# Kernel optimization log

Hardware: AMD Instinct MI355X
Metric: run time of the kernel (lower is better)

## Reference

```python
import jax, jax.numpy as jnp
import numpy as np

B, S, D = 2, 8192, 1024
H, DK, DV = 8, 64, 64
DH = 4096
SEG = 2048
NSEG = S // SEG
EPS = 1e-5


def setup_inputs() -> dict:
    key = jax.random.key(0)
    ks = jax.random.split(key, 9)
    g = lambda k, shp, sc: jax.random.normal(k, shp, jnp.float32) * sc
    return {
        "x": g(ks[0], (B, S, D), 1.0),
        "Wq": g(ks[1], (D, H * DK), 0.02),
        "Wk": g(ks[2], (D, H * DK), 0.02),
        "Wv": g(ks[3], (D, H * DV), 0.02),
        "Wo": g(ks[4], (H * DV, D), 0.02),
        "betas": g(ks[5], (1, H, 1, DV), 1.0),
        "W1": g(ks[6], (D, DH), 0.02),
        "b1": jnp.zeros((DH,), jnp.float32),
        "W2": g(ks[7], (DH, D), 0.02),
        "b2": jnp.zeros((D,), jnp.float32),
        "ln_g": jnp.ones((D,), jnp.float32),
        "ln_b": jnp.zeros((D,), jnp.float32),
    }


def _compressive_memory(x, Wq, Wk, Wv, Wo, betas):
    # project and split heads: (B, H, S, d)
    q = (x @ Wq).reshape(B, S, H, DK).transpose(0, 2, 1, 3)
    k = (x @ Wk).reshape(B, S, H, DK).transpose(0, 2, 1, 3)
    v = (x @ Wv).reshape(B, S, H, DV).transpose(0, 2, 1, 3)

    # chunk into segments: (NSEG, B, H, SEG, d)
    seg = lambda t, d: t.reshape(B, H, NSEG, SEG, d).transpose(2, 0, 1, 3, 4)
    qs, ks_, vs = seg(q, DK), seg(k, DK), seg(v, DV)

    mem0 = jnp.zeros((B, H, DK, DV), jnp.float32)
    z0 = jnp.ones((B, H, DK, 1), jnp.float32) / DK
    causal_mask = jnp.tril(jnp.ones((SEG, SEG), bool))
    scale = np.float32(1.0 / np.sqrt(DK))
    gate = jax.nn.sigmoid(betas)  # (1, H, 1, DV)

    def step(carry, inp):
        mem, z = carry
        qi, ki, vi = inp  # (B, H, SEG, d)
        sq = jax.nn.elu(qi) + 1.0
        sk = jax.nn.elu(ki) + 1.0
        # memory retrieval (uses state from previous segments)
        att_mem = (sq @ mem) / (sq @ z)  # (B, H, SEG, DV)
        # local causal SDP attention within the segment
        scores = jnp.einsum('bhqd,bhkd->bhqk', qi, ki) * scale
        scores = jnp.where(causal_mask, scores, -jnp.inf)
        att_dot = jax.nn.softmax(scores, axis=-1) @ vi
        # linear memory update
        mem = mem + jnp.einsum('bhsd,bhsv->bhdv', sk, vi)
        z = z + sk.sum(axis=-2, keepdims=True).transpose(0, 1, 3, 2)
        att = gate * att_mem + (1.0 - gate) * att_dot
        return (mem, z), att

    _, atts = jax.lax.scan(step, (mem0, z0), (qs, ks_, vs))
    # (NSEG, B, H, SEG, DV) -> (B, S, H*DV)
    att = atts.transpose(1, 0, 3, 2, 4).reshape(B, S, H * DV)
    return att @ Wo


def reference(x, Wq, Wk, Wv, Wo, betas, W1, b1, W2, b2, ln_g, ln_b):
    a = _compressive_memory(x, Wq, Wk, Wv, Wo, betas)
    h = jax.nn.gelu(a @ W1 + b1, approximate=False) @ W2 + b2
    y = h + x
    mu = y.mean(axis=-1, keepdims=True)
    var = ((y - mu) ** 2).mean(axis=-1, keepdims=True)
    return (y - mu) / jnp.sqrt(var + EPS) * ln_g + ln_b
```

## Files before the change

### kernel.cpp

```cpp
#include <hip/hip_runtime.h>
#include <hip/hip_bf16.h>
#include <math.h>

#define B_    2
#define S_    8192
#define D_    1024
#define H_N   8
#define DK_   64
#define DV_   64
#define DH_   4096
#define SEG_  2048
#define NSEG_ 4
#define EPS_  1e-5f
#define LDQKV 1536

typedef __hip_bfloat16 bf16;
typedef unsigned int u32;
typedef __attribute__((ext_vector_type(8))) short bf16x8;
typedef __attribute__((ext_vector_type(4))) float f32x4;

union bvec { bf16x8 v; bf16 e[8]; };

template <typename T> __device__ inline T from_f(float v);
template <> __device__ inline float from_f<float>(float v) { return v; }
template <> __device__ inline bf16  from_f<bf16>(float v)  { return __float2bfloat16(v); }

__device__ __forceinline__ void gld_lds16(const bf16* g, bf16* l) {
    __builtin_amdgcn_global_load_lds(
        (const __attribute__((address_space(1))) u32*)g,
        (__attribute__((address_space(3))) u32*)l, 16, 0, 0);
}

__device__ inline float elu1(float x) { return x > 0.f ? x + 1.f : __expf(x); }

template <int EPI, typename CT>
__global__ __launch_bounds__(512, 2) void gemm256(
    const bf16* __restrict__ A, const bf16* __restrict__ BT, CT* __restrict__ C,
    const float* __restrict__ bias, const float* __restrict__ resid,
    int M, int N, int K)
{
    __shared__ bf16 L[4][16384];
    const int t    = threadIdx.x;
    const int lane = t & 63;
    const int w    = t >> 6;
    const int la   = lane & 15;
    const int g    = lane >> 4;

    const int nx  = gridDim.x;
    const int nwg = nx * gridDim.y;
    const int lin = blockIdx.y * nx + blockIdx.x;
    const int swz = (lin & 7) * (nwg >> 3) + (lin >> 3);
    const int by  = swz / nx, bx = swz - by * nx;

    const int m0 = by * 256, n0 = bx * 256;
    const int wm = w >> 2, wn = w & 3;

    f32x4 acc[8][4];
    #pragma unroll
    for (int m = 0; m < 8; m++)
        #pragma unroll
        for (int n = 0; n < 4; n++) {
            f32x4 z4 = {0.f, 0.f, 0.f, 0.f};
            acc[m][n] = z4;
        }

    const bf16* Aw = A  + (size_t)(m0 + w * 32) * K;
    const bf16* Bw = BT + (size_t)(n0 + w * 32) * K;
    const int rl = lane >> 2;
    const int co = (((lane & 3) ^ ((lane >> 3) & 3))) * 8;

    const int nt = K >> 5;

    auto stage = [&](int kt) {
        const int buf = kt & 3;
        const int k0 = kt << 5;
        #pragma unroll
        for (int i = 0; i < 2; i++) {
            gld_lds16(Aw + (size_t)(i * 16 + rl) * K + k0 + co,
                      &L[buf][(w * 32 + i * 16) * 32]);
            gld_lds16(Bw + (size_t)(i * 16 + rl) * K + k0 + co,
                      &L[buf][8192 + (w * 32 + i * 16) * 32]);
        }
    };

    stage(0);
    stage(1);
    asm volatile("s_waitcnt vmcnt(4)" ::: "memory");
    __builtin_amdgcn_s_barrier();

    for (int kt = 0; kt < nt; kt++) {
        const int buf = kt & 3;
        if (kt + 2 < nt) stage(kt + 2);

        const bf16* Ab_ = &L[buf][0];
        const bf16* Bb_ = &L[buf][8192];
        const int rsw = (la >> 1) & 3;
        bf16x8 af[8], bg[4];
        #pragma unroll
        for (int m = 0; m < 8; m++) {
            int row = wm * 128 + m * 16 + la;
            af[m] = *(const bf16x8*)&Ab_[row * 32 + 8 * (g ^ rsw)];
        }
        #pragma unroll
        for (int n = 0; n < 4; n++) {
            int row = wn * 64 + n * 16 + la;
            bg[n] = *(const bf16x8*)&Bb_[row * 32 + 8 * (g ^ rsw)];
        }

        __builtin_amdgcn_s_setprio(1);
        #pragma unroll
        for (int m = 0; m < 8; m++)
            #pragma unroll
            for (int n = 0; n < 4; n++)
                acc[m][n] = __builtin_amdgcn_mfma_f32_16x16x32_bf16(
                    af[m], bg[n], acc[m][n], 0, 0, 0);
        __builtin_amdgcn_s_setprio(0);

        if (kt + 1 < nt) {
            if (kt + 2 < nt) asm volatile("s_waitcnt vmcnt(4)" ::: "memory");
            else             asm volatile("s_waitcnt vmcnt(0)" ::: "memory");
            __builtin_amdgcn_sched_barrier(0);
            __builtin_amdgcn_s_barrier();
        }
    }

    const int row0 = m0 + wm * 128 + g * 4;
    const int col0 = n0 + wn * 64 + la;
    #pragma unroll
    for (int n = 0; n < 4; n++) {
        const int col = col0 + n * 16;
        const float bj = (EPI >= 2) ? bias[col] : 0.f;
        #pragma unroll
        for (int m = 0; m < 8; m++) {
            #pragma unroll
            for (int r = 0; r < 4; r++) {
                const int row = row0 + m * 16 + r;
                float v = acc[m][n][r];
                if (EPI >= 2) v += bj;
                if (EPI == 2) v = 0.5f * v * (1.0f + erff(v * 0.70710678118654752f));
                if (EPI == 3) v += resid[(size_t)row * N + col];
                C[(size_t)row * N + col] = from_f<CT>(v);
            }
        }
    }
}

__global__ __launch_bounds__(256) void castx_k(const float* __restrict__ X,
                                               bf16* __restrict__ Y)
{
    size_t i = ((size_t)blockIdx.x * 256 + threadIdx.x) * 4;
    float4 v = *(const float4*)(X + i);
    union { bf16 b[4]; unsigned long long u; } o;
    o.b[0] = __float2bfloat16(v.x);
    o.b[1] = __float2bfloat16(v.y);
    o.b[2] = __float2bfloat16(v.z);
    o.b[3] = __float2bfloat16(v.w);
    *(unsigned long long*)(Y + i) = o.u;
}

__global__ __launch_bounds__(256) void transcast_k(const float* __restrict__ W,
                                                   bf16* __restrict__ WT, int K, int N)
{
    __shared__ float tile[32][33];
    const int n0 = blockIdx.x * 32, k0 = blockIdx.y * 32;
    const int tx = threadIdx.x & 31, ty = threadIdx.x >> 5;
    #pragma unroll
    for (int i = 0; i < 32; i += 8)
        tile[ty + i][tx] = W[(size_t)(k0 + ty + i) * N + n0 + tx];
    __syncthreads();
    #pragma unroll
    for (int i = 0; i < 32; i += 8)
        WT[(size_t)(n0 + ty + i) * K + k0 + tx] = __float2bfloat16(tile[tx][ty + i]);
}

__global__ __launch_bounds__(256) void vtrans_k(const bf16* __restrict__ V,
                                                bf16* __restrict__ Vt)
{
    __shared__ bf16 t_[64 * 64];
    const int t = threadIdx.x;
    const int sblk = blockIdx.x & 127;
    const int b = blockIdx.x >> 7;
    const int h = blockIdx.y;
    const bf16* src = V + ((size_t)b * S_ + sblk * 64) * LDQKV + h * 64;
    #pragma unroll
    for (int k = 0; k < 2; k++) {
        int e = t + k * 256;
        int r = e >> 3, c8 = (e & 7) * 8;
        *(bf16x8*)&t_[r * 64 + c8] = *(const bf16x8*)&src[(size_t)r * LDQKV + c8];
    }
    __syncthreads();
    const int dv = t & 63, s0 = (t >> 6) * 16;
    bf16* dst = Vt + ((size_t)(b * 8 + h) * 64 + dv) * (size_t)S_ + sblk * 64 + s0;
    bvec o0, o1;
    #pragma unroll
    for (int i = 0; i < 8; i++) {
        o0.e[i] = t_[(s0 + i) * 64 + dv];
        o1.e[i] = t_[(s0 + 8 + i) * 64 + dv];
    }
    *(bf16x8*)dst = o0.v;
    *(bf16x8*)(dst + 8) = o1.v;
}

__global__ __launch_bounds__(256) void memseg_k(
    const bf16* __restrict__ Kg, const bf16* __restrict__ Vg,
    float* __restrict__ MP, float* __restrict__ ZP)
{
    __shared__ float Ks[64][65];
    __shared__ float Vs[64][65];
    const int t = threadIdx.x, tx = t & 15, ty = t >> 4;
    const int sb = blockIdx.x;
    const int seg = sb >> 4, bh = sb & 15;
    const int b = bh >> 3, h = bh & 7;
    const int chunk = blockIdx.y;
    const size_t base = ((size_t)b * S_ + (size_t)seg * SEG_ + (size_t)chunk * 512) * LDQKV + h * 64;

    float acc[4][4] = {};
    float zacc[4]   = {};
    for (int st = 0; st < 8; st++) {
        #pragma unroll
        for (int kk = 0; kk < 2; kk++) {
            int e = t + kk * 256;
            int r = e >> 3, c8 = (e & 7) * 8;
            size_t go = base + ((size_t)st * 64 + r) * LDQKV + c8;
            bvec kv_, vv_;
            kv_.v = *(const bf16x8*)&Kg[go];
            vv_.v = *(const bf16x8*)&Vg[go];
            #pragma unroll
            for (int i = 0; i < 8; i++) {
                Ks[r][c8 + i] = elu1(__bfloat162float(kv_.e[i]));
                Vs[r][c8 + i] = __bfloat162float(vv_.e[i]);
            }
        }
        __syncthreads();
        for (int s = 0; s < 64; s++) {
            float a4[4], v4[4];
            #pragma unroll
            for (int i = 0; i < 4; i++) a4[i] = Ks[s][ty * 4 + i];
            #pragma unroll
            for (int j = 0; j < 4; j++) v4[j] = Vs[s][tx * 4 + j];
            #pragma unroll
            for (int i = 0; i < 4; i++)
                #pragma unroll
                for (int j = 0; j < 4; j++)
                    acc[i][j] += a4[i] * v4[j];
        }
        #pragma unroll
        for (int ii = 0; ii < 4; ii++) {
            int s = tx + ii * 16;
            #pragma unroll
            for (int i = 0; i < 4; i++) zacc[i] += Ks[s][ty * 4 + i];
        }
        __syncthreads();
    }
    const int slot = (seg * 4 + chunk) * 16 + bh;
    #pragma unroll
    for (int i = 0; i < 4; i++)
        #pragma unroll
        for (int j = 0; j < 4; j++)
            MP[(size_t)slot * 4096 + (ty * 4 + i) * 64 + tx * 4 + j] = acc[i][j];
    #pragma unroll
    for (int i = 0; i < 4; i++) {
        float zz = zacc[i];
        #pragma unroll
        for (int mk = 1; mk < 16; mk <<= 1) zz += __shfl_xor(zz, mk);
        if (tx == 0) ZP[slot * 64 + ty * 4 + i] = zz;
    }
}

__global__ __launch_bounds__(256) void prefix_k(
    const float* __restrict__ MP, const float* __restrict__ ZP,
    bf16* __restrict__ MST, float* __restrict__ ZS)
{
    const int bh = blockIdx.x, t = threadIdx.x;
    for (int e = t; e < 4096; e += 256) {
        int dk = e >> 6, dv = e & 63;
        float s = 0.f;
        #pragma unroll
        for (int slot = 0; slot < 16; slot++) {
            if ((slot & 3) == 0)
                MST[(size_t)((slot >> 2) * 16 + bh) * 4096 + dv * 64 + dk] = __float2bfloat16(s);
            s += MP[(size_t)(slot * 16 + bh) * 4096 + e];
        }
    }
    if (t < 64) {
        float s = 1.0f / DK_;
        #pragma unroll
        for (int slot = 0; slot < 16; slot++) {
            if ((slot & 3) == 0) ZS[((slot >> 2) * 16 + bh) * 64 + t] = s;
            s += ZP[(slot * 16 + bh) * 64 + t];
        }
    }
}

template <int NG>
__device__ __forceinline__ void stageT(const bf16* gsrc, size_t stride, bf16* lds,
                                       int wave, int lane)
{
    #pragma unroll
    for (int ii = 0; ii < NG; ii++) {
        int i = wave * NG + ii;
        gld_lds16(gsrc + (size_t)(8 * i + (lane >> 3)) * stride
                        + (size_t)(((lane & 7) ^ (lane >> 3)) * 8),
                  lds + i * 512);
    }
}

__device__ __forceinline__ bf16x8 ldsw128(const bf16* base, int row, int colE)
{
    int off = row * 128 + ((colE * 2) ^ ((row & 7) << 4));
    return *(const bf16x8*)((const char*)base + off);
}

__global__ __launch_bounds__(256) void attn_k(
    const bf16* __restrict__ Qg, const bf16* __restrict__ Kg, const bf16* __restrict__ Vt,
    const bf16* __restrict__ MsT, const float* __restrict__ ZS,
    const float* __restrict__ betas, bf16* __restrict__ att)
{
    __shared__ bf16 KT[2][4096];
    __shared__ bf16 VTs[2][4096];
    __shared__ bf16 QP[8192];
    __shared__ float Zsm[64];

    const int t    = threadIdx.x;
    const int lane = t & 63;
    const int w    = t >> 6;
    const int la   = lane & 15;
    const int g    = lane >> 4;
    const int qt   = (int)gridDim.x - 1 - (int)blockIdx.x;
    const int bh   = blockIdx.y;
    const int seg  = blockIdx.z;
    const int b    = bh >> 3, h = bh & 7;

    const size_t srow = (size_t)b * S_ + (size_t)seg * SEG_;
    const bf16* qp  = Qg + (srow + (size_t)qt * 128) * LDQKV + h * 64;
    const bf16* kp  = Kg + srow * LDQKV + h * 64;
    const bf16* vtp = Vt + (size_t)bh * 64 * (size_t)S_ + (size_t)seg * SEG_;

    stageT<4>(qp, LDQKV, QP, w, lane);
    stageT<2>(kp, LDQKV, KT[0], w, lane);
    stageT<2>(vtp, S_, VTs[0], w, lane);
    if (t < 64) Zsm[t] = ZS[(seg * 16 + bh) * 64 + t];
    __syncthreads();

    bf16x8 aq[2][2];
    #pragma unroll
    for (int st = 0; st < 2; st++)
        #pragma unroll
        for (int s = 0; s < 2; s++)
            aq[st][s] = ldsw128(QP, w * 32 + st * 16 + la, s * 32 + g * 8);

    float m_[2] = {-1e30f, -1e30f};
    float l_[2] = {0.f, 0.f};
    f32x4 Oa[2][4];
    #pragma unroll
    for (int st = 0; st < 2; st++)
        #pragma unroll
        for (int j = 0; j < 4; j++) { f32x4 z4 = {0.f,0.f,0.f,0.f}; Oa[st][j] = z4; }

    const int jtmax = 2 * qt + 1;
    int cur = 0;
    for (int jt = 0; jt <= jtmax; jt++, cur ^= 1) {
        if (jt < jtmax) {
            stageT<2>(kp + (size_t)(jt + 1) * 64 * LDQKV, LDQKV, KT[cur ^ 1], w, lane);
            stageT<2>(vtp + (size_t)(jt + 1) * 64, S_, VTs[cur ^ 1], w, lane);
        }

        bf16x8 kf[2][4];
        #pragma unroll
        for (int s = 0; s < 2; s++)
            #pragma unroll
            for (int j = 0; j < 4; j++)
                kf[s][j] = ldsw128(KT[cur], j * 16 + la, s * 32 + g * 8);

        const int jtkv = jt * 64;
        #pragma unroll
        for (int st = 0; st < 2; st++) {
            f32x4 sc[4];
            #pragma unroll
            for (int j = 0; j < 4; j++) { f32x4 z4 = {0.f,0.f,0.f,0.f}; sc[j] = z4; }
            #pragma unroll
            for (int j = 0; j < 4; j++) {
                sc[j] = __builtin_amdgcn_mfma_f32_16x16x32_bf16(kf[0][j], aq[st][0], sc[j], 0, 0, 0);
                sc[j] = __builtin_amdgcn_mfma_f32_16x16x32_bf16(kf[1][j], aq[st][1], sc[j], 0, 0, 0);
            }

            const int q_abs = qt * 128 + w * 32 + st * 16 + la;
            float sv[4][4];
            float mx = -1e30f;
            #pragma unroll
            for (int j = 0; j < 4; j++)
                #pragma unroll
                for (int r = 0; r < 4; r++) {
                    float v = sc[j][r] * 0.125f;
                    int kv = jtkv + j * 16 + g * 4 + r;
                    v = (kv <= q_abs) ? v : -1e30f;
                    sv[j][r] = v;
                    mx = fmaxf(mx, v);
                }
            mx = fmaxf(mx, __shfl_xor(mx, 16));
            mx = fmaxf(mx, __shfl_xor(mx, 32));
            float mnew = fmaxf(m_[st], mx);
            float corr = __expf(m_[st] - mnew);
            float rs = 0.f;
            #pragma unroll
            for (int j = 0; j < 4; j++)
                #pragma unroll
                for (int r = 0; r < 4; r++) {
                    float p = __expf(sv[j][r] - mnew);
                    sv[j][r] = p;
                    rs += p;
                }
            rs += __shfl_xor(rs, 16);
            rs += __shfl_xor(rs, 32);
            l_[st] = l_[st] * corr + rs;
            m_[st] = mnew;

            const int R = w * 32 + st * 16 + la;
            #pragma unroll
            for (int j = 0; j < 4; j++) {
                union { bf16 e[4]; uint2 u; } pk;
                #pragma unroll
                for (int r = 0; r < 4; r++) pk.e[r] = __float2bfloat16(sv[j][r]);
                int off = R * 128 + ((j * 32 + g * 8) ^ ((la & 7) << 4));
                *(uint2*)((char*)QP + off) = pk.u;
            }

            #pragma unroll
            for (int r = 0; r < 4; r++) {
                float corr_r = __shfl(corr, (lane & 48) | (g * 4 + r));
                #pragma unroll
                for (int j = 0; j < 4; j++) Oa[st][j][r] *= corr_r;
            }
        }

        asm volatile("s_waitcnt lgkmcnt(0)" ::: "memory");
        __builtin_amdgcn_sched_barrier(0);

        bf16x8 bv[2][4];
        #pragma unroll
        for (int s = 0; s < 2; s++)
            #pragma unroll
            for (int j = 0; j < 4; j++)
                bv[s][j] = ldsw128(VTs[cur], j * 16 + la, s * 32 + g * 8);
        #pragma unroll
        for (int st = 0; st < 2; st++) {
            bf16x8 ap0 = ldsw128(QP, w * 32 + st * 16 + la, g * 8);
            bf16x8 ap1 = ldsw128(QP, w * 32 + st * 16 + la, 32 + g * 8);
            #pragma unroll
            for (int j = 0; j < 4; j++) {
                Oa[st][j] = __builtin_amdgcn_mfma_f32_16x16x32_bf16(ap0, bv[0][j], Oa[st][j], 0, 0, 0);
                Oa[st][j] = __builtin_amdgcn_mfma_f32_16x16x32_bf16(ap1, bv[1][j], Oa[st][j], 0, 0, 0);
            }
        }
        __syncthreads();
    }

    stageT<2>(MsT + (size_t)(seg * 16 + bh) * 4096, 64, KT[0], w, lane);
    __syncthreads();

    bf16x8 sq[2][2];
    float den[2] = {0.f, 0.f};
    #pragma unroll
    for (int st = 0; st < 2; st++) {
        #pragma unroll
        for (int s = 0; s < 2; s++) {
            bvec in, outv;
            in.v = aq[st][s];
            #pragma unroll
            for (int e = 0; e < 8; e++) {
                float f = elu1(__bfloat162float(in.e[e]));
                outv.e[e] = __float2bfloat16(f);
                den[st] += f * Zsm[s * 32 + g * 8 + e];
            }
            sq[st][s] = outv.v;
        }
        den[st] += __shfl_xor(den[st], 16);
        den[st] += __shfl_xor(den[st], 32);
    }

    bf16x8 bm[2][4];
    #pragma unroll
    for (int s = 0; s < 2; s++)
        #pragma unroll
        for (int j = 0; j < 4; j++)
            bm[s][j] = ldsw128(KT[0], j * 16 + la, s * 32 + g * 8);

    float gate[4];
    #pragma unroll
    for (int j = 0; j < 4; j++)
        gate[j] = 1.f / (1.f + __expf(-betas[h * 64 + j * 16 + la]));

    #pragma unroll
    for (int st = 0; st < 2; st++) {
        f32x4 num[4];
        #pragma unroll
        for (int j = 0; j < 4; j++) { f32x4 z4 = {0.f,0.f,0.f,0.f}; num[j] = z4; }
        #pragma unroll
        for (int j = 0; j < 4; j++) {
            num[j] = __builtin_amdgcn_mfma_f32_16x16x32_bf16(sq[st][0], bm[0][j], num[j], 0, 0, 0);
            num[j] = __builtin_amdgcn_mfma_f32_16x16x32_bf16(sq[st][1], bm[1][j], num[j], 0, 0, 0);
        }
        #pragma unroll
        for (int r = 0; r < 4; r++) {
            float den_r = __shfl(den[st], (lane & 48) | (g * 4 + r));
            float l_r   = __shfl(l_[st],  (lane & 48) | (g * 4 + r));
            float linv  = 1.f / l_r;
            float dinv  = 1.f / den_r;
            size_t orow = srow + (size_t)qt * 128 + w * 32 + st * 16 + g * 4 + r;
            #pragma unroll
            for (int j = 0; j < 4; j++) {
                float am = num[j][r] * dinv;
                float ad = Oa[st][j][r] * linv;
                att[orow * 512 + h * 64 + j * 16 + la] =
                    __float2bfloat16(gate[j] * am + (1.f - gate[j]) * ad);
            }
        }
    }
}

__global__ __launch_bounds__(256) void ln_k(
    const float* __restrict__ Y, const float* __restrict__ g,
    const float* __restrict__ bta, float* __restrict__ out)
{
    const int row = blockIdx.x;
    const float* yp = Y + (size_t)row * D_;
    const int t = threadIdx.x;
    float v[4];
    float s = 0.f, s2 = 0.f;
    #pragma unroll
    for (int i = 0; i < 4; i++) {
        v[i] = yp[t + i * 256];
        s += v[i]; s2 += v[i] * v[i];
    }
    #pragma unroll
    for (int mk = 1; mk < 64; mk <<= 1) {
        s  += __shfl_xor(s, mk);
        s2 += __shfl_xor(s2, mk);
    }
    __shared__ float ss[4], ss2[4];
    int w = t >> 6;
    if ((t & 63) == 0) { ss[w] = s; ss2[w] = s2; }
    __syncthreads();
    s  = ss[0] + ss[1] + ss[2] + ss[3];
    s2 = ss2[0] + ss2[1] + ss2[2] + ss2[3];
    float mu   = s / D_;
    float var  = s2 / D_ - mu * mu;
    float rstd = rsqrtf(var + EPS_);
    #pragma unroll
    for (int i = 0; i < 4; i++) {
        int c = t + i * 256;
        out[(size_t)row * D_ + c] = (v[i] - mu) * rstd * g[c] + bta[c];
    }
}

extern "C" void kernel_launch(void* const* d_in, const int* in_sizes, int n_in,
                              void* d_out, int out_size, void* d_ws, size_t ws_size,
                              hipStream_t stream)
{
    const float* x     = (const float*)d_in[0];
    const float* Wq    = (const float*)d_in[1];
    const float* Wk    = (const float*)d_in[2];
    const float* Wv    = (const float*)d_in[3];
    const float* Wo    = (const float*)d_in[4];
    const float* betas = (const float*)d_in[5];
    const float* W1    = (const float*)d_in[6];
    const float* b1    = (const float*)d_in[7];
    const float* W2    = (const float*)d_in[8];
    const float* b2    = (const float*)d_in[9];
    const float* lng   = (const float*)d_in[10];
    const float* lnb   = (const float*)d_in[11];
    float* out = (float*)d_out;

    const int M = B_ * S_;
    char* base = (char*)d_ws;
    const size_t MB = 1024 * 1024;

    bf16*  Ab    = (bf16*)(base);
    bf16*  Hb    = (bf16*)(base + 32 * MB);
    bf16*  Xbf   = (bf16*)(base + 32 * MB);
    bf16*  QKV   = (bf16*)(base + 64 * MB);
    bf16*  Vt    = (bf16*)(base + 112 * MB);
    bf16*  ATT   = (bf16*)(base + 128 * MB);
    bf16*  WqkvT = (bf16*)(base + 160 * MB);
    bf16*  WoT   = (bf16*)(base + 163 * MB);
    bf16*  W1T   = (bf16*)(base + 164 * MB);
    bf16*  W2T   = (bf16*)(base + 172 * MB);
    float* MP    = (float*)(base + 180 * MB);
    bf16*  MST   = (bf16*)(base + 184 * MB);
    float* ZP    = (float*)(base + 185 * MB);
    float* ZS    = (float*)(base + 185 * MB + 256 * 1024);

    dim3 blk(256);
    dim3 blk512(512);

    castx_k<<<dim3((M * D_) / 1024), blk, 0, stream>>>(x, Xbf);
    transcast_k<<<dim3(512 / 32, 1024 / 32), blk, 0, stream>>>(Wq, WqkvT, 1024, 512);
    transcast_k<<<dim3(512 / 32, 1024 / 32), blk, 0, stream>>>(Wk, WqkvT + 512 * 1024, 1024, 512);
    transcast_k<<<dim3(512 / 32, 1024 / 32), blk, 0, stream>>>(Wv, WqkvT + 1024 * 1024, 1024, 512);
    transcast_k<<<dim3(1024 / 32, 512 / 32), blk, 0, stream>>>(Wo, WoT, 512, 1024);
    transcast_k<<<dim3(4096 / 32, 1024 / 32), blk, 0, stream>>>(W1, W1T, 1024, 4096);
    transcast_k<<<dim3(1024 / 32, 4096 / 32), blk, 0, stream>>>(W2, W2T, 4096, 1024);

    gemm256<0, bf16><<<dim3(1536 / 256, M / 256), blk512, 0, stream>>>(
        Xbf, WqkvT, QKV, nullptr, nullptr, M, 1536, 1024);

    vtrans_k<<<dim3(256, 8), blk, 0, stream>>>(QKV + 1024, Vt);

    memseg_k<<<dim3(NSEG_ * 16, 4), blk, 0, stream>>>(QKV + 512, QKV + 1024, MP, ZP);
    prefix_k<<<dim3(16), blk, 0, stream>>>(MP, ZP, MST, ZS);

    attn_k<<<dim3(SEG_ / 128, 16, NSEG_), blk, 0, stream>>>(
        QKV, QKV + 512, Vt, MST, ZS, betas, ATT);

    gemm256<0, bf16><<<dim3(1024 / 256, M / 256), blk512, 0, stream>>>(
        ATT, WoT, Ab, nullptr, nullptr, M, 1024, 512);
    gemm256<2, bf16><<<dim3(4096 / 256, M / 256), blk512, 0, stream>>>(
        Ab, W1T, Hb, b1, nullptr, M, 4096, 1024);
    gemm256<3, float><<<dim3(1024 / 256, M / 256), blk512, 0, stream>>>(
        Hb, W2T, out, b2, x, M, 1024, 4096);

    ln_k<<<dim3(M), blk, 0, stream>>>(out, lng, lnb, out);
}
```

Measured before the change: 714.9 us.

## Switch GEMM to 64-wide K tiles with double buffering and XOR swizzle

The 256x256 GEMM now stages K tiles of 64 instead of 32, so a main-loop iteration covers twice as much work per barrier. The LDS ring drops from four buffers to two, with prefetch depth one, and the swizzle becomes an 8-chunk XOR on 128-byte rows. Fragment loads are split into halves to keep register pressure down. The aim is to halve barrier and waitcnt overhead per FLOP, at the cost of a shallower prefetch that may expose more global-load latency.

```diff
diff --git a/kernel.cpp b/kernel.cpp
--- a/kernel.cpp
+++ b/kernel.cpp
@@ -39,7 +39,7 @@
     const float* __restrict__ bias, const float* __restrict__ resid,
     int M, int N, int K)
 {
-    __shared__ bf16 L[4][16384];
+    __shared__ bf16 L[2][32768];
     const int t    = threadIdx.x;
     const int lane = t & 63;
     const int w    = t >> 6;
@@ -66,61 +66,66 @@
 
     const bf16* Aw = A  + (size_t)(m0 + w * 32) * K;
     const bf16* Bw = BT + (size_t)(n0 + w * 32) * K;
-    const int rl = lane >> 2;
-    const int co = (((lane & 3) ^ ((lane >> 3) & 3))) * 8;
-
-    const int nt = K >> 5;
+    const int sr = lane >> 3;
+    const int sc = ((lane & 7) ^ sr) * 8;
+
+    const int nt = K >> 6;
 
     auto stage = [&](int kt) {
-        const int buf = kt & 3;
-        const int k0 = kt << 5;
-        #pragma unroll
-        for (int i = 0; i < 2; i++) {
-            gld_lds16(Aw + (size_t)(i * 16 + rl) * K + k0 + co,
-                      &L[buf][(w * 32 + i * 16) * 32]);
-            gld_lds16(Bw + (size_t)(i * 16 + rl) * K + k0 + co,
-                      &L[buf][8192 + (w * 32 + i * 16) * 32]);
+        const int buf = kt & 1;
+        const size_t k0 = (size_t)kt << 6;
+        #pragma unroll
+        for (int i = 0; i < 4; i++) {
+            gld_lds16(Aw + (size_t)(i * 8 + sr) * K + k0 + sc,
+                      &L[buf][(w * 32 + i * 8) * 64]);
+            gld_lds16(Bw + (size_t)(i * 8 + sr) * K + k0 + sc,
+                      &L[buf][16384 + (w * 32 + i * 8) * 64]);
         }
     };
 
+    auto rd = [&](const bf16* base, int row, int chunk) -> bf16x8 {
+        return *(const bf16x8*)((const char*)base + row * 128 + ((chunk ^ (row & 7)) << 4));
+    };
+
     stage(0);
-    stage(1);
-    asm volatile("s_waitcnt vmcnt(4)" ::: "memory");
+    asm volatile("s_waitcnt vmcnt(0)" ::: "memory");
+    __builtin_amdgcn_sched_barrier(0);
     __builtin_amdgcn_s_barrier();
+    __builtin_amdgcn_sched_barrier(0);
 
     for (int kt = 0; kt < nt; kt++) {
-        const int buf = kt & 3;
-        if (kt + 2 < nt) stage(kt + 2);
-
-        const bf16* Ab_ = &L[buf][0];
-        const bf16* Bb_ = &L[buf][8192];
-        const int rsw = (la >> 1) & 3;
-        bf16x8 af[8], bg[4];
-        #pragma unroll
-        for (int m = 0; m < 8; m++) {
-            int row = wm * 128 + m * 16 + la;
-            af[m] = *(const bf16x8*)&Ab_[row * 32 + 8 * (g ^ rsw)];
-        }
-        #pragma unroll
-        for (int n = 0; n < 4; n++) {
-            int row = wn * 64 + n * 16 + la;
-            bg[n] = *(const bf16x8*)&Bb_[row * 32 + 8 * (g ^ rsw)];
-        }
-
-        __builtin_amdgcn_s_setprio(1);
-        #pragma unroll
-        for (int m = 0; m < 8; m++)
+        const bf16* Abuf = &L[kt & 1][0];
+        const bf16* Bbuf = &L[kt & 1][16384];
+        if (kt + 1 < nt) stage(kt + 1);
+
+        #pragma unroll
+        for (int ks = 0; ks < 2; ks++) {
+            bf16x8 bg[4];
             #pragma unroll
             for (int n = 0; n < 4; n++)
-                acc[m][n] = __builtin_amdgcn_mfma_f32_16x16x32_bf16(
-                    af[m], bg[n], acc[m][n], 0, 0, 0);
-        __builtin_amdgcn_s_setprio(0);
+                bg[n] = rd(Bbuf, wn * 64 + n * 16 + la, ks * 4 + g);
+            #pragma unroll
+            for (int mh = 0; mh < 2; mh++) {
+                bf16x8 af[4];
+                #pragma unroll
+                for (int m = 0; m < 4; m++)
+                    af[m] = rd(Abuf, wm * 128 + mh * 64 + m * 16 + la, ks * 4 + g);
+                __builtin_amdgcn_s_setprio(1);
+                #pragma unroll
+                for (int m = 0; m < 4; m++)
+                    #pragma unroll
+                    for (int n = 0; n < 4; n++)
+                        acc[mh * 4 + m][n] = __builtin_amdgcn_mfma_f32_16x16x32_bf16(
+                            af[m], bg[n], acc[mh * 4 + m][n], 0, 0, 0);
+                __builtin_amdgcn_s_setprio(0);
+            }
+        }
 
         if (kt + 1 < nt) {
-            if (kt + 2 < nt) asm volatile("s_waitcnt vmcnt(4)" ::: "memory");
-            else             asm volatile("s_waitcnt vmcnt(0)" ::: "memory");
+            asm volatile("s_waitcnt vmcnt(0)" ::: "memory");
             __builtin_amdgcn_sched_barrier(0);
             __builtin_amdgcn_s_barrier();
+            __builtin_amdgcn_sched_barrier(0);
         }
     }
 
@@ -470,7 +475,7 @@
             for (int e = 0; e < 8; e++) {
                 float f = elu1(__bfloat162float(in.e[e]));
                 outv.e[e] = __float2bfloat16(f);
-                den[st] += f * Zsm[s * 32 + g * 8 + e];
+                den[st] += f * Zsm[s * 32 + 8 * g + e];
             }
             sq[st][s] = outv.v;
         }
```

New measurement: 702.4 us. No clear change (-1.7%).
